# Performance work log

Hardware: AMD Instinct MI355X
Metric: run time of the kernel (lower is better)

Reference implementation:

```python
import jax, jax.numpy as jnp
import numpy as np

U, I, E, T = 60000, 30000, 64, 2000
N = U + I
ADJ_NNZ = 1_600_000
UI_NNZ = 800_000
TAGS_PER_ITEM = 4


def setup_inputs() -> dict:
    key = jax.random.key(0)
    ks = jax.random.split(key, 8)
    # LightGCN normalized adjacency in COO form (values already normalized offline)
    adj_rows = jax.random.randint(ks[0], (ADJ_NNZ,), 0, N, dtype=jnp.int32)
    adj_cols = jax.random.randint(ks[1], (ADJ_NNZ,), 0, N, dtype=jnp.int32)
    adj_vals = jax.random.uniform(ks[2], (ADJ_NNZ,), dtype=jnp.float32) * 0.01
    # Item-tag incidence H: 4 distinct tags per item (binary incidence, no duplicates)
    items_np = np.repeat(np.arange(I, dtype=np.int32), TAGS_PER_ITEM)
    tags_np = ((np.arange(I, dtype=np.int64)[:, None] * 7919 + np.arange(TAGS_PER_ITEM)[None, :] * 131) % T).astype(np.int32).reshape(-1)
    h_items = jnp.asarray(items_np)
    h_tags = jnp.asarray(tags_np)
    # Row-normalized user-item interaction matrix (D_u^-1 @ trn_mat) in COO form
    ui_rows = jax.random.randint(ks[3], (UI_NNZ,), 0, U, dtype=jnp.int32)
    ui_cols = jax.random.randint(ks[4], (UI_NNZ,), 0, I, dtype=jnp.int32)
    ui_vals = jax.random.uniform(ks[5], (UI_NNZ,), dtype=jnp.float32) * 0.01
    return {
        'user_embeds': jax.random.normal(ks[6], (U, E), dtype=jnp.float32) * 0.1,
        'item_embeds': jax.random.normal(jax.random.fold_in(ks[6], 1), (I, E), dtype=jnp.float32) * 0.1,
        'hypergraph_user_embeds': jax.random.normal(ks[7], (U, E), dtype=jnp.float32) * 0.1,
        'hypergraph_item_embeds': jax.random.normal(jax.random.fold_in(ks[7], 1), (I, E), dtype=jnp.float32) * 0.1,
        'adj_rows': adj_rows, 'adj_cols': adj_cols, 'adj_vals': adj_vals,
        'h_items': h_items, 'h_tags': h_tags,
        'ui_rows': ui_rows, 'ui_cols': ui_cols, 'ui_vals': ui_vals,
        'layer_num': 3,
    }


def _spmm(rows, cols, vals, x, n):
    # y[r] += vals[e] * x[cols[e]] for each edge e with rows[e]==r  (t.spmm)
    return jax.ops.segment_sum(vals[:, None] * x[cols], rows, num_segments=n)


def reference(user_embeds, item_embeds, hypergraph_user_embeds, hypergraph_item_embeds,
              adj_rows, adj_cols, adj_vals, h_items, h_tags, ui_rows, ui_cols, ui_vals,
              layer_num):
    ones = jnp.ones(h_items.shape[0], dtype=user_embeds.dtype)
    # B: hyperedge (tag) degree; D: item degree; zero degrees clamped to 1
    B = jax.ops.segment_sum(ones, h_tags, num_segments=T)
    D = jax.ops.segment_sum(ones, h_items, num_segments=I)
    B_inv = 1.0 / jnp.where(B == 0, 1.0, B)
    D_inv = 1.0 / jnp.where(D == 0, 1.0, D)

    def hconv(x):  # D^-1 H B^-1 H^T x, never materializing the item x item adjacency
        y = jax.ops.segment_sum(x[h_items], h_tags, num_segments=T) * B_inv[:, None]
        z = jax.ops.segment_sum(y[h_tags], h_items, num_segments=I)
        return z * D_inv[:, None]

    # LightGCN propagation: sum of all layer embeddings (layer 0 included)
    cur = jnp.concatenate([user_embeds, item_embeds], axis=0)  # [N, E]
    acc = cur
    for _ in range(layer_num):
        cur = _spmm(adj_rows, adj_cols, adj_vals, cur, N)
        acc = acc + cur

    # Hypergraph propagation on items
    hcur = hypergraph_item_embeds
    hacc = hcur
    for _ in range(layer_num):
        hcur = hconv(hcur)
        hacc = hacc + hcur

    # Hypergraph user embeds: own params + degree-normalized sum of interacted items
    hg_user = hypergraph_user_embeds + _spmm(ui_rows, ui_cols, ui_vals, hacc, U)

    return acc[:U], acc[U:], hg_user, hacc
```

## Files before the change

kernel.cpp:

```cpp
#include <hip/hip_runtime.h>

#define E 64
#define TQ 16
#define RPB 256
#define RPB_SHIFT 8
#define NBMAX 1024
#define CHUNK_C 4096
#define CHUNK_P 4096
#define FP8_SCALE 512.0f
#define FP8_INV   (1.0f / 512.0f)

static inline int nblk(long n, int bs) { return (int)((n + bs - 1) / bs); }


__device__ __forceinline__ unsigned short f2bf(float f) {
    unsigned u = __float_as_uint(f);
    u += 0x7FFF + ((u >> 16) & 1);
    return (unsigned short)(u >> 16);
}
__device__ __forceinline__ float bf2f(unsigned short h) {
    return __uint_as_float((unsigned)h << 16);
}
__device__ __forceinline__ int f2v15(float f) {
    unsigned u = __float_as_uint(f);
    u += 0x7FFF + ((u >> 16) & 1);
    return (int)((u >> 16) & 0x7FFF);
}
__device__ __forceinline__ float v15f(int p) {
    return __uint_as_float(((unsigned)p >> 17) << 16);
}
__device__ __forceinline__ int pack_fp8x4(float4 v) {
    int w = __builtin_amdgcn_cvt_pk_fp8_f32(v.x, v.y, 0, false);
    w = __builtin_amdgcn_cvt_pk_fp8_f32(v.z, v.w, w, true);
    return w;
}


__global__ void __launch_bounds__(512)
k_count_cvt(const int* __restrict__ adj_rows, int nadj,
            const int* __restrict__ ui_rows, int nui,
            const int* __restrict__ h_tags,
            int* __restrict__ bucket_cnt, int OFF_UI, int OFF_TAG, int NB, int ET,
            const float4* __restrict__ ua, const float4* __restrict__ ub,
            int splitv4, int* __restrict__ xf8, int ncvt, int CB) {
    __shared__ int h4[4][NBMAX];
    if ((int)blockIdx.x < CB) {
        for (int b = threadIdx.x; b < 4 * NBMAX; b += 512) ((int*)h4)[b] = 0;
        __syncthreads();
        int c = (threadIdx.x >> 4) & 3;
        int start = blockIdx.x * CHUNK_C;
        int end = start + CHUNK_C; if (end > ET) end = ET;
        for (int i = start + (int)threadIdx.x; i < end; i += 512) {
            int row;
            if (i < nadj) row = adj_rows[i];
            else if (i < nadj + nui) row = OFF_UI + ui_rows[i - nadj];
            else row = OFF_TAG + h_tags[i - nadj - nui];
            atomicAdd(&h4[c][row >> RPB_SHIFT], 1);
        }
        __syncthreads();
        for (int b = threadIdx.x; b < NB; b += 512) {
            int tot = h4[0][b] + h4[1][b] + h4[2][b] + h4[3][b];
            if (tot) atomicAdd(&bucket_cnt[b], tot);
        }
    } else {
        int i = ((int)blockIdx.x - CB) * 512 + threadIdx.x;
        if (i < ncvt) {
            float4 v = (i < splitv4) ? ua[i] : ub[i - splitv4];
            v.x *= FP8_SCALE; v.y *= FP8_SCALE; v.z *= FP8_SCALE; v.w *= FP8_SCALE;
            xf8[i] = pack_fp8x4(v);
        }
    }
}


__global__ void __launch_bounds__(1024)
k_scan_nb(const int* __restrict__ cnt, int* __restrict__ base, int* __restrict__ bcur,
          int* __restrict__ rp, int M, int NB, int ET) {
    __shared__ int sh[1024];
    int tid = threadIdx.x;
    int v = (tid < NB) ? cnt[tid] : 0;
    sh[tid] = v;
    __syncthreads();
    for (int off = 1; off < 1024; off <<= 1) {
        int t = (tid >= off) ? sh[tid - off] : 0;
        __syncthreads();
        sh[tid] += t;
        __syncthreads();
    }
    if (tid < NB) {
        int excl = sh[tid] - v;
        base[tid] = excl;
        bcur[tid] = excl;
        if (tid == NB - 1) base[NB] = sh[tid];
    }
    if (tid == 0) rp[M] = ET;
}


__global__ void __launch_bounds__(512)
k_partition(const int* __restrict__ adj_rows, const int* __restrict__ adj_cols,
            const float* __restrict__ adj_vals, int nadj,
            const int* __restrict__ ui_rows, const int* __restrict__ ui_cols,
            const float* __restrict__ ui_vals, int nui,
            const int* __restrict__ h_tags, const int* __restrict__ h_items,
            int* __restrict__ bcur, int2* __restrict__ staged,
            int OFF_UI, int OFF_TAG, int NB, int ET) {
    __shared__ int h4[4][NBMAX];
    for (int b = threadIdx.x; b < 4 * NBMAX; b += 512) ((int*)h4)[b] = 0;
    __syncthreads();

    int c = (threadIdx.x >> 4) & 3;
    int start = blockIdx.x * CHUNK_P;

    int rowA[8], colA[8], vbA[8];
    #pragma unroll
    for (int k = 0; k < 8; ++k) {
        int i = start + k * 512 + (int)threadIdx.x;
        int row = -1, col = 0, vb = 0;
        if (i < ET) {
            if (i < nadj) {
                row = adj_rows[i]; col = adj_cols[i]; vb = f2v15(adj_vals[i]);
            } else if (i < nadj + nui) {
                int j = i - nadj;
                row = OFF_UI + ui_rows[j]; col = ui_cols[j]; vb = f2v15(ui_vals[j]);
            } else {
                int j = i - nadj - nui;
                row = OFF_TAG + h_tags[j]; col = h_items[j]; vb = 0;
            }
            atomicAdd(&h4[c][row >> RPB_SHIFT], 1);
        }
        rowA[k] = row; colA[k] = col; vbA[k] = vb;
    }
    __syncthreads();

    for (int b = threadIdx.x; b < NB; b += 512) {
        int c0 = h4[0][b], c1 = h4[1][b], c2 = h4[2][b], c3 = h4[3][b];
        int tot = c0 + c1 + c2 + c3;
        if (tot) {
            int g = atomicAdd(&bcur[b], tot);
            h4[0][b] = g;
            h4[1][b] = g + c0;
            h4[2][b] = g + c0 + c1;
            h4[3][b] = g + c0 + c1 + c2;
        }
    }
    __syncthreads();

    #pragma unroll
    for (int k = 0; k < 8; ++k) {
        if (rowA[k] >= 0) {
            int b = rowA[k] >> RPB_SHIFT;
            int pos = atomicAdd(&h4[c][b], 1);
            staged[pos] = make_int2(((rowA[k] & (RPB - 1)) << 17) | colA[k], vbA[k]);
        }
    }
}


__global__ void __launch_bounds__(512)
k_bucket_csr(const int2* __restrict__ staged, const int* __restrict__ bbase,
             int* __restrict__ rp, int* __restrict__ pool, int M) {
    __shared__ int h4[4][RPB];
    __shared__ int scn[RPB];
    int b = blockIdx.x;
    int s0 = bbase[b], s1 = bbase[b + 1];
    for (int i = threadIdx.x; i < 4 * RPB; i += 512) ((int*)h4)[i] = 0;
    __syncthreads();
    int c = (threadIdx.x >> 4) & 3;
    for (int e = s0 + (int)threadIdx.x; e < s1; e += 512) {
        int lrow = ((unsigned)staged[e].x) >> 17;
        atomicAdd(&h4[c][lrow], 1);
    }
    __syncthreads();
    int tot = (threadIdx.x < RPB)
        ? h4[0][threadIdx.x] + h4[1][threadIdx.x] + h4[2][threadIdx.x] + h4[3][threadIdx.x] : 0;
    if (threadIdx.x < RPB) scn[threadIdx.x] = tot;
    __syncthreads();
    for (int off = 1; off < RPB; off <<= 1) {
        int t = 0;
        if (threadIdx.x < RPB && (int)threadIdx.x >= off) t = scn[threadIdx.x - off];
        __syncthreads();
        if (threadIdx.x < RPB) scn[threadIdx.x] += t;
        __syncthreads();
    }
    int row0 = b << RPB_SHIFT;
    if (threadIdx.x < RPB) {
        int excl = s0 + scn[threadIdx.x] - tot;
        if (row0 + (int)threadIdx.x < M) rp[row0 + threadIdx.x] = excl;
        int c0 = h4[0][threadIdx.x], c1 = h4[1][threadIdx.x], c2 = h4[2][threadIdx.x];
        h4[0][threadIdx.x] = excl;
        h4[1][threadIdx.x] = excl + c0;
        h4[2][threadIdx.x] = excl + c0 + c1;
        h4[3][threadIdx.x] = excl + c0 + c1 + c2;
    }
    __syncthreads();
    for (int e = s0 + (int)threadIdx.x; e < s1; e += 512) {
        int2 ed = staged[e];
        int lrow = ((unsigned)ed.x) >> 17;
        int pos = atomicAdd(&h4[c][lrow], 1);
        pool[pos] = (ed.y << 17) | (ed.x & 0x1FFFF);
    }
}


__device__ __forceinline__ void spmm_body(const int* __restrict__ rp,
                                          const int* __restrict__ pool,
                                          const int* __restrict__ xf8,
                                          int* __restrict__ yf8, int n, int bid) {
    int gid = bid * 256 + (int)threadIdx.x;
    int row = gid >> 4;
    if (row >= n) return;
    int q = gid & 15;
    int s0 = rp[row], s1 = rp[row + 1];
    float4 s = make_float4(0.f, 0.f, 0.f, 0.f);
    int e = s0;
    for (; e + 4 <= s1; e += 4) {
        int p0 = pool[e], p1 = pool[e + 1], p2 = pool[e + 2], p3 = pool[e + 3];
        int w0 = xf8[(long)(p0 & 0x1FFFF) * TQ + q];
        int w1 = xf8[(long)(p1 & 0x1FFFF) * TQ + q];
        int w2 = xf8[(long)(p2 & 0x1FFFF) * TQ + q];
        int w3 = xf8[(long)(p3 & 0x1FFFF) * TQ + q];
        float v0 = v15f(p0), v1 = v15f(p1), v2 = v15f(p2), v3 = v15f(p3);
        s.x += v0 * __builtin_amdgcn_cvt_f32_fp8(w0, 0);
        s.y += v0 * __builtin_amdgcn_cvt_f32_fp8(w0, 1);
        s.z += v0 * __builtin_amdgcn_cvt_f32_fp8(w0, 2);
        s.w += v0 * __builtin_amdgcn_cvt_f32_fp8(w0, 3);
        s.x += v1 * __builtin_amdgcn_cvt_f32_fp8(w1, 0);
        s.y += v1 * __builtin_amdgcn_cvt_f32_fp8(w1, 1);
        s.z += v1 * __builtin_amdgcn_cvt_f32_fp8(w1, 2);
        s.w += v1 * __builtin_amdgcn_cvt_f32_fp8(w1, 3);
        s.x += v2 * __builtin_amdgcn_cvt_f32_fp8(w2, 0);
        s.y += v2 * __builtin_amdgcn_cvt_f32_fp8(w2, 1);
        s.z += v2 * __builtin_amdgcn_cvt_f32_fp8(w2, 2);
        s.w += v2 * __builtin_amdgcn_cvt_f32_fp8(w2, 3);
        s.x += v3 * __builtin_amdgcn_cvt_f32_fp8(w3, 0);
        s.y += v3 * __builtin_amdgcn_cvt_f32_fp8(w3, 1);
        s.z += v3 * __builtin_amdgcn_cvt_f32_fp8(w3, 2);
        s.w += v3 * __builtin_amdgcn_cvt_f32_fp8(w3, 3);
    }
    for (; e < s1; ++e) {
        int p0 = pool[e];
        int w0 = xf8[(long)(p0 & 0x1FFFF) * TQ + q];
        float v0 = v15f(p0);
        s.x += v0 * __builtin_amdgcn_cvt_f32_fp8(w0, 0);
        s.y += v0 * __builtin_amdgcn_cvt_f32_fp8(w0, 1);
        s.z += v0 * __builtin_amdgcn_cvt_f32_fp8(w0, 2);
        s.w += v0 * __builtin_amdgcn_cvt_f32_fp8(w0, 3);
    }
    yf8[(long)row * TQ + q] = pack_fp8x4(s);
}

__device__ __forceinline__ void tag_hop_body(const int* __restrict__ rp, int rp_off,
                                             const int* __restrict__ pool,
                                             const float* __restrict__ x,
                                             float* __restrict__ y, int ntags, int bid) {
    int t = (bid * 256 + (int)threadIdx.x) >> 6;
    if (t >= ntags) return;
    int lane = threadIdx.x & 63;
    int q = lane & 15;
    int g = lane >> 4;
    int s0 = rp[rp_off + t], s1 = rp[rp_off + t + 1];
    float4 s = make_float4(0.f, 0.f, 0.f, 0.f);
    for (int e = s0 + g; e < s1; e += 4) {
        int it = pool[e] & 0x1FFFF;
        float4 xv = ((const float4*)x)[(long)it * TQ + q];
        s.x += xv.x; s.y += xv.y; s.z += xv.z; s.w += xv.w;
    }
    s.x += __shfl_xor(s.x, 16, 64); s.y += __shfl_xor(s.y, 16, 64);
    s.z += __shfl_xor(s.z, 16, 64); s.w += __shfl_xor(s.w, 16, 64);
    s.x += __shfl_xor(s.x, 32, 64); s.y += __shfl_xor(s.y, 32, 64);
    s.z += __shfl_xor(s.z, 32, 64); s.w += __shfl_xor(s.w, 32, 64);
    if (g == 0) {
        int b = s1 - s0;
        float binv = (b > 0) ? (1.f / (float)b) : 1.f;
        s.x *= binv; s.y *= binv; s.z *= binv; s.w *= binv;
        ((float4*)y)[(long)t * TQ + q] = s;
    }
}

__device__ __forceinline__ void tag_g_body(const int* __restrict__ rp, int rp_off,
                                           const int* __restrict__ pool,
                                           const int* __restrict__ tags, int K,
                                           const float* __restrict__ yin,
                                           const float* __restrict__ yprev,
                                           float* __restrict__ yout, int ntags, int bid) {
    int t = (bid * 256 + (int)threadIdx.x) >> 6;
    if (t >= ntags) return;
    int lane = threadIdx.x & 63;
    int q = lane & 15;
    int g = lane >> 4;
    int s0 = rp[rp_off + t], s1 = rp[rp_off + t + 1];
    float4 s = make_float4(0.f, 0.f, 0.f, 0.f);
    if (K == 4) {
        for (int e = s0 + g; e < s1; e += 4) {
            int it = pool[e] & 0x1FFFF;
            int4 t4 = ((const int4*)tags)[it];
            float4 a0 = ((const float4*)yin)[(long)t4.x * TQ + q];
            float4 a1 = ((const float4*)yin)[(long)t4.y * TQ + q];
            float4 a2 = ((const float4*)yin)[(long)t4.z * TQ + q];
            float4 a3 = ((const float4*)yin)[(long)t4.w * TQ + q];
            s.x += (a0.x + a1.x) + (a2.x + a3.x);
            s.y += (a0.y + a1.y) + (a2.y + a3.y);
            s.z += (a0.z + a1.z) + (a2.z + a3.z);
            s.w += (a0.w + a1.w) + (a2.w + a3.w);
        }
    } else {
        for (int e = s0 + g; e < s1; e += 4) {
            int it = pool[e] & 0x1FFFF;
            for (int k = 0; k < K; ++k) {
                int tt = tags[(long)it * K + k];
                float4 a = ((const float4*)yin)[(long)tt * TQ + q];
                s.x += a.x; s.y += a.y; s.z += a.z; s.w += a.w;
            }
        }
    }
    s.x += __shfl_xor(s.x, 16, 64); s.y += __shfl_xor(s.y, 16, 64);
    s.z += __shfl_xor(s.z, 16, 64); s.w += __shfl_xor(s.w, 16, 64);
    s.x += __shfl_xor(s.x, 32, 64); s.y += __shfl_xor(s.y, 32, 64);
    s.z += __shfl_xor(s.z, 32, 64); s.w += __shfl_xor(s.w, 32, 64);
    if (g == 0) {
        int b = s1 - s0;
        float dinv = 1.f / (float)K;
        float f = (b > 0) ? (dinv / (float)b) : 0.f;
        s.x *= f; s.y *= f; s.z *= f; s.w *= f;
        long o = (long)t * TQ + q;
        if (yprev) {
            float4 p1 = ((const float4*)yprev)[o];
            float4 p2 = ((const float4*)yin)[o];
            s.x += p1.x + p2.x; s.y += p1.y + p2.y;
            s.z += p1.z + p2.z; s.w += p1.w + p2.w;
        }
        ((float4*)yout)[o] = s;
    }
}

__device__ __forceinline__ void items_body(const int* __restrict__ tags, int K,
                                           const float* __restrict__ ysum,
                                           const float* __restrict__ init,
                                           float* __restrict__ hacc,
                                           ushort4* __restrict__ hacc_bf,
                                           int nitems, int bid) {
    int gid = bid * 256 + (int)threadIdx.x;
    int i = gid >> 4;
    if (i >= nitems) return;
    int q = gid & 15;
    float4 s = make_float4(0.f, 0.f, 0.f, 0.f);
    if (K == 4) {
        int4 t4 = ((const int4*)tags)[i];
        float4 y0 = ((const float4*)ysum)[(long)t4.x * TQ + q];
        float4 y1 = ((const float4*)ysum)[(long)t4.y * TQ + q];
        float4 y2 = ((const float4*)ysum)[(long)t4.z * TQ + q];
        float4 y3 = ((const float4*)ysum)[(long)t4.w * TQ + q];
        s.x = (y0.x + y1.x) + (y2.x + y3.x);
        s.y = (y0.y + y1.y) + (y2.y + y3.y);
        s.z = (y0.z + y1.z) + (y2.z + y3.z);
        s.w = (y0.w + y1.w) + (y2.w + y3.w);
    } else {
        for (int k = 0; k < K; ++k) {
            int tt = tags[(long)i * K + k];
            float4 yv = ((const float4*)ysum)[(long)tt * TQ + q];
            s.x += yv.x; s.y += yv.y; s.z += yv.z; s.w += yv.w;
        }
    }
    float dinv = 1.f / (float)K;
    s.x *= dinv; s.y *= dinv; s.z *= dinv; s.w *= dinv;
    long o = (long)i * TQ + q;
    float4 a = ((const float4*)init)[o];
    a.x += s.x; a.y += s.y; a.z += s.z; a.w += s.w;
    ((float4*)hacc)[o] = a;
    ushort4 hb;
    hb.x = f2bf(a.x); hb.y = f2bf(a.y); hb.z = f2bf(a.z); hb.w = f2bf(a.w);
    hacc_bf[o] = hb;
}


__global__ void __launch_bounds__(256)
k_spmm_tag(const int* __restrict__ rp, const int* __restrict__ pool,
           const int* __restrict__ xf8, int* __restrict__ yf8, int n, int SB,
           int rp_off, const float* __restrict__ xtag, float* __restrict__ y1,
           int ntags) {
    if ((int)blockIdx.x < SB)
        spmm_body(rp, pool, xf8, yf8, n, blockIdx.x);
    else
        tag_hop_body(rp, rp_off, pool, xtag, y1, ntags, (int)blockIdx.x - SB);
}

__global__ void __launch_bounds__(256)
k_spmm_g(const int* __restrict__ rp, const int* __restrict__ pool,
         const int* __restrict__ xf8, int* __restrict__ yf8, int n, int SB,
         int rp_off, const int* __restrict__ tags, int K,
         const float* __restrict__ yin, const float* __restrict__ yprev,
         float* __restrict__ yout, int ntags) {
    if ((int)blockIdx.x < SB)
        spmm_body(rp, pool, xf8, yf8, n, blockIdx.x);
    else
        tag_g_body(rp, rp_off, pool, tags, K, yin, yprev, yout, ntags,
                   (int)blockIdx.x - SB);
}

__global__ void __launch_bounds__(256)
k_final_items(const float4* __restrict__ ua, const float4* __restrict__ ub,
              int splitv4, const int* __restrict__ l1, const int* __restrict__ l2,
              const int* __restrict__ l3, float4* __restrict__ acc, int n4, int FSB,
              const int* __restrict__ tags, int K, const float* __restrict__ ysum,
              const float* __restrict__ hyper_item, float* __restrict__ hacc,
              ushort4* __restrict__ hacc_bf, int nitems) {
    if ((int)blockIdx.x < FSB) {
        int i = (int)blockIdx.x * 256 + threadIdx.x;
        if (i >= n4) return;
        float4 a = (i < splitv4) ? ua[i] : ub[i - splitv4];
        int w1 = l1[i], w2 = l2[i], w3 = l3[i];
        a.x += (__builtin_amdgcn_cvt_f32_fp8(w1, 0) + __builtin_amdgcn_cvt_f32_fp8(w2, 0)
                + __builtin_amdgcn_cvt_f32_fp8(w3, 0)) * FP8_INV;
        a.y += (__builtin_amdgcn_cvt_f32_fp8(w1, 1) + __builtin_amdgcn_cvt_f32_fp8(w2, 1)
                + __builtin_amdgcn_cvt_f32_fp8(w3, 1)) * FP8_INV;
        a.z += (__builtin_amdgcn_cvt_f32_fp8(w1, 2) + __builtin_amdgcn_cvt_f32_fp8(w2, 2)
                + __builtin_amdgcn_cvt_f32_fp8(w3, 2)) * FP8_INV;
        a.w += (__builtin_amdgcn_cvt_f32_fp8(w1, 3) + __builtin_amdgcn_cvt_f32_fp8(w2, 3)
                + __builtin_amdgcn_cvt_f32_fp8(w3, 3)) * FP8_INV;
        acc[i] = a;
    } else {
        items_body(tags, K, ysum, hyper_item, hacc, hacc_bf, nitems,
                   (int)blockIdx.x - FSB);
    }
}


__global__ void k_csr_spmm_base_bf(const int* __restrict__ rp, int rp_off,
                                   const int* __restrict__ pool,
                                   const ushort4* __restrict__ xbf,
                                   const float* __restrict__ base,
                                   float* __restrict__ out, int n) {
    int gid = blockIdx.x * blockDim.x + threadIdx.x;
    int row = gid >> 4;
    if (row >= n) return;
    int q = gid & 15;
    int s0 = rp[rp_off + row], s1 = rp[rp_off + row + 1];
    float4 s = make_float4(0.f, 0.f, 0.f, 0.f);
    int e = s0;
    for (; e + 4 <= s1; e += 4) {
        int p0 = pool[e], p1 = pool[e + 1], p2 = pool[e + 2], p3 = pool[e + 3];
        ushort4 h0 = xbf[(long)(p0 & 0x1FFFF) * TQ + q];
        ushort4 h1 = xbf[(long)(p1 & 0x1FFFF) * TQ + q];
        ushort4 h2 = xbf[(long)(p2 & 0x1FFFF) * TQ + q];
        ushort4 h3 = xbf[(long)(p3 & 0x1FFFF) * TQ + q];
        float v0 = v15f(p0), v1 = v15f(p1), v2 = v15f(p2), v3 = v15f(p3);
        s.x += v0 * bf2f(h0.x); s.y += v0 * bf2f(h0.y);
        s.z += v0 * bf2f(h0.z); s.w += v0 * bf2f(h0.w);
        s.x += v1 * bf2f(h1.x); s.y += v1 * bf2f(h1.y);
        s.z += v1 * bf2f(h1.z); s.w += v1 * bf2f(h1.w);
        s.x += v2 * bf2f(h2.x); s.y += v2 * bf2f(h2.y);
        s.z += v2 * bf2f(h2.z); s.w += v2 * bf2f(h2.w);
        s.x += v3 * bf2f(h3.x); s.y += v3 * bf2f(h3.y);
        s.z += v3 * bf2f(h3.z); s.w += v3 * bf2f(h3.w);
    }
    for (; e < s1; ++e) {
        int p0 = pool[e];
        ushort4 h0 = xbf[(long)(p0 & 0x1FFFF) * TQ + q];
        float v0 = v15f(p0);
        s.x += v0 * bf2f(h0.x); s.y += v0 * bf2f(h0.y);
        s.z += v0 * bf2f(h0.z); s.w += v0 * bf2f(h0.w);
    }
    long o = (long)row * TQ + q;
    float4 bv = ((const float4*)base)[o];
    bv.x += s.x; bv.y += s.y; bv.z += s.z; bv.w += s.w;
    ((float4*)out)[o] = bv;
}


extern "C" void kernel_launch(void* const* d_in, const int* in_sizes, int n_in,
                              void* d_out, int out_size, void* d_ws, size_t ws_size,
                              hipStream_t stream) {
    const float* user_embeds = (const float*)d_in[0];
    const float* item_embeds = (const float*)d_in[1];
    const float* hyper_user  = (const float*)d_in[2];
    const float* hyper_item  = (const float*)d_in[3];
    const int*   adj_rows    = (const int*)d_in[4];
    const int*   adj_cols    = (const int*)d_in[5];
    const float* adj_vals    = (const float*)d_in[6];
    const int*   h_items     = (const int*)d_in[7];
    const int*   h_tags      = (const int*)d_in[8];
    const int*   ui_rows     = (const int*)d_in[9];
    const int*   ui_cols     = (const int*)d_in[10];
    const float* ui_vals     = (const float*)d_in[11];

    const int U = in_sizes[0] / E;
    const int I = in_sizes[1] / E;
    const int N = U + I;
    const int ADJ = in_sizes[4];
    const int NH  = in_sizes[7];
    const int UI  = in_sizes[9];
    const int K   = NH / I;
    const int T   = 2000;
    const int ET  = ADJ + UI + NH;

    const int OFF_UI  = (N + RPB - 1) & ~(RPB - 1);
    const int OFF_TAG = (OFF_UI + U + RPB - 1) & ~(RPB - 1);
    const int M   = OFF_TAG + T;
    const int NB  = (M + RPB - 1) >> RPB_SHIFT;

    float* out     = (float*)d_out;
    float* acc     = out;
    float* hg_user = out + (size_t)N * E;
    float* hacc    = hg_user + (size_t)U * E;

    char* ws = (char*)d_ws;
    auto alloc = [&](size_t bytes) { char* p = ws; ws += (bytes + 255) & ~(size_t)255; return p; };

    int*  xf0 = (int*)alloc((size_t)N * TQ * sizeof(int));
    int*  xf1 = (int*)alloc((size_t)N * TQ * sizeof(int));
    int*  xf2 = (int*)alloc((size_t)N * TQ * sizeof(int));
    int*  xf3 = (int*)alloc((size_t)N * TQ * sizeof(int));
    int2* staged = (int2*)alloc((size_t)ET * sizeof(int2));
    float* y1      = (float*)alloc((size_t)T * E * sizeof(float));
    float* y2      = (float*)alloc((size_t)T * E * sizeof(float));
    float* ys      = (float*)alloc((size_t)T * E * sizeof(float));
    unsigned short* hacc_bf = (unsigned short*)alloc((size_t)I * E * sizeof(unsigned short));
    int*   pool    = (int*)alloc((size_t)ET * sizeof(int));
    int*   rp      = (int*)alloc((size_t)(M + 1) * sizeof(int));
    int*   bcnt    = (int*)alloc((size_t)NBMAX * sizeof(int));
    int*   bbase   = (int*)alloc((size_t)(NBMAX + 1) * sizeof(int));
    int*   bcur    = (int*)alloc((size_t)NBMAX * sizeof(int));

    const int BS = 256;
    const int TAG_BLOCKS = nblk((long)T * 64, 256);
    const int CB  = nblk(ET, CHUNK_C);
    const int CVB = nblk((long)N * TQ, 512);
    const int SB  = nblk((long)N * TQ, BS);
    const int FSB = nblk((long)N * TQ, BS);
    const int IB  = nblk((long)I * TQ, BS);

    hipMemsetAsync(bcnt, 0, (size_t)NB * sizeof(int), stream);
    k_count_cvt<<<CB + CVB, 512, 0, stream>>>(
        adj_rows, ADJ, ui_rows, UI, h_tags, bcnt, OFF_UI, OFF_TAG, NB, ET,
        (const float4*)user_embeds, (const float4*)item_embeds, U * TQ,
        xf0, N * TQ, CB);
    k_scan_nb<<<1, 1024, 0, stream>>>(bcnt, bbase, bcur, rp, M, NB, ET);
    k_partition<<<nblk(ET, CHUNK_P), 512, 0, stream>>>(
        adj_rows, adj_cols, adj_vals, ADJ, ui_rows, ui_cols, ui_vals, UI,
        h_tags, h_items, bcur, staged, OFF_UI, OFF_TAG, NB, ET);
    k_bucket_csr<<<NB, 512, 0, stream>>>(staged, bbase, rp, pool, M);

    k_spmm_tag<<<SB + TAG_BLOCKS, BS, 0, stream>>>(
        rp, pool, xf0, xf1, N, SB, OFF_TAG, hyper_item, y1, T);
    k_spmm_g<<<SB + TAG_BLOCKS, BS, 0, stream>>>(
        rp, pool, xf1, xf2, N, SB, OFF_TAG, h_tags, K, y1, nullptr, y2, T);
    k_spmm_g<<<SB + TAG_BLOCKS, BS, 0, stream>>>(
        rp, pool, xf2, xf3, N, SB, OFF_TAG, h_tags, K, y2, y1, ys, T);

    k_final_items<<<FSB + IB, BS, 0, stream>>>(
        (const float4*)user_embeds, (const float4*)item_embeds, U * TQ,
        xf1, xf2, xf3, (float4*)acc, N * TQ, FSB,
        h_tags, K, ys, hyper_item, hacc, (ushort4*)hacc_bf, I);

    k_csr_spmm_base_bf<<<nblk((long)U * TQ, BS), BS, 0, stream>>>(
        rp, OFF_UI, pool, (const ushort4*)hacc_bf, hyper_user, hg_user, U);
}
```

Measured before the change: 333.8 us.

## Fuse final LightGCN layer with accumulation and unroll gather loops by eight

The third adjacency SpMM layer now accumulates the input embeddings plus the two earlier FP8 layers and its own fp32 result straight into the output. This removes the xf3 intermediate and its write and re-read in a separate final kernel. The item hypergraph step becomes its own kernel. The FP8 and BF16 gather loops are also unrolled to eight edges to keep more loads in flight, at the cost of higher register pressure. The last layer now stays in fp32 instead of being rounded through FP8, which slightly changes the numerics.

Result: no change. 331.8 us (-0.6%).

```diff
diff --git a/kernel.cpp b/kernel.cpp
--- a/kernel.cpp
+++ b/kernel.cpp
@@ -203,6 +203,50 @@
 }
 
 
+#define FP8_ACC(ss, ww, vv)                                               \
+    ss.x += vv * __builtin_amdgcn_cvt_f32_fp8(ww, 0);                     \
+    ss.y += vv * __builtin_amdgcn_cvt_f32_fp8(ww, 1);                     \
+    ss.z += vv * __builtin_amdgcn_cvt_f32_fp8(ww, 2);                     \
+    ss.w += vv * __builtin_amdgcn_cvt_f32_fp8(ww, 3);
+
+__device__ __forceinline__ float4 spmm_sum(const int* __restrict__ pool,
+                                           const int* __restrict__ xf8,
+                                           int s0, int s1, int q) {
+    float4 s = make_float4(0.f, 0.f, 0.f, 0.f);
+    int e = s0;
+    for (; e + 8 <= s1; e += 8) {
+        int p0 = pool[e],     p1 = pool[e + 1], p2 = pool[e + 2], p3 = pool[e + 3];
+        int p4 = pool[e + 4], p5 = pool[e + 5], p6 = pool[e + 6], p7 = pool[e + 7];
+        int w0 = xf8[(long)(p0 & 0x1FFFF) * TQ + q];
+        int w1 = xf8[(long)(p1 & 0x1FFFF) * TQ + q];
+        int w2 = xf8[(long)(p2 & 0x1FFFF) * TQ + q];
+        int w3 = xf8[(long)(p3 & 0x1FFFF) * TQ + q];
+        int w4 = xf8[(long)(p4 & 0x1FFFF) * TQ + q];
+        int w5 = xf8[(long)(p5 & 0x1FFFF) * TQ + q];
+        int w6 = xf8[(long)(p6 & 0x1FFFF) * TQ + q];
+        int w7 = xf8[(long)(p7 & 0x1FFFF) * TQ + q];
+        FP8_ACC(s, w0, v15f(p0)); FP8_ACC(s, w1, v15f(p1));
+        FP8_ACC(s, w2, v15f(p2)); FP8_ACC(s, w3, v15f(p3));
+        FP8_ACC(s, w4, v15f(p4)); FP8_ACC(s, w5, v15f(p5));
+        FP8_ACC(s, w6, v15f(p6)); FP8_ACC(s, w7, v15f(p7));
+    }
+    for (; e + 4 <= s1; e += 4) {
+        int p0 = pool[e], p1 = pool[e + 1], p2 = pool[e + 2], p3 = pool[e + 3];
+        int w0 = xf8[(long)(p0 & 0x1FFFF) * TQ + q];
+        int w1 = xf8[(long)(p1 & 0x1FFFF) * TQ + q];
+        int w2 = xf8[(long)(p2 & 0x1FFFF) * TQ + q];
+        int w3 = xf8[(long)(p3 & 0x1FFFF) * TQ + q];
+        FP8_ACC(s, w0, v15f(p0)); FP8_ACC(s, w1, v15f(p1));
+        FP8_ACC(s, w2, v15f(p2)); FP8_ACC(s, w3, v15f(p3));
+    }
+    for (; e < s1; ++e) {
+        int p0 = pool[e];
+        int w0 = xf8[(long)(p0 & 0x1FFFF) * TQ + q];
+        FP8_ACC(s, w0, v15f(p0));
+    }
+    return s;
+}
+
 __device__ __forceinline__ void spmm_body(const int* __restrict__ rp,
                                           const int* __restrict__ pool,
                                           const int* __restrict__ xf8,
@@ -211,43 +255,35 @@
     int row = gid >> 4;
     if (row >= n) return;
     int q = gid & 15;
-    int s0 = rp[row], s1 = rp[row + 1];
-    float4 s = make_float4(0.f, 0.f, 0.f, 0.f);
-    int e = s0;
-    for (; e + 4 <= s1; e += 4) {
-        int p0 = pool[e], p1 = pool[e + 1], p2 = pool[e + 2], p3 = pool[e + 3];
-        int w0 = xf8[(long)(p0 & 0x1FFFF) * TQ + q];
-        int w1 = xf8[(long)(p1 & 0x1FFFF) * TQ + q];
-        int w2 = xf8[(long)(p2 & 0x1FFFF) * TQ + q];
-        int w3 = xf8[(long)(p3 & 0x1FFFF) * TQ + q];
-        float v0 = v15f(p0), v1 = v15f(p1), v2 = v15f(p2), v3 = v15f(p3);
-        s.x += v0 * __builtin_amdgcn_cvt_f32_fp8(w0, 0);
-        s.y += v0 * __builtin_amdgcn_cvt_f32_fp8(w0, 1);
-        s.z += v0 * __builtin_amdgcn_cvt_f32_fp8(w0, 2);
-        s.w += v0 * __builtin_amdgcn_cvt_f32_fp8(w0, 3);
-        s.x += v1 * __builtin_amdgcn_cvt_f32_fp8(w1, 0);
-        s.y += v1 * __builtin_amdgcn_cvt_f32_fp8(w1, 1);
-        s.z += v1 * __builtin_amdgcn_cvt_f32_fp8(w1, 2);
-        s.w += v1 * __builtin_amdgcn_cvt_f32_fp8(w1, 3);
-        s.x += v2 * __builtin_amdgcn_cvt_f32_fp8(w2, 0);
-        s.y += v2 * __builtin_amdgcn_cvt_f32_fp8(w2, 1);
-        s.z += v2 * __builtin_amdgcn_cvt_f32_fp8(w2, 2);
-        s.w += v2 * __builtin_amdgcn_cvt_f32_fp8(w2, 3);
-        s.x += v3 * __builtin_amdgcn_cvt_f32_fp8(w3, 0);
-        s.y += v3 * __builtin_amdgcn_cvt_f32_fp8(w3, 1);
-        s.z += v3 * __builtin_amdgcn_cvt_f32_fp8(w3, 2);
-        s.w += v3 * __builtin_amdgcn_cvt_f32_fp8(w3, 3);
-    }
-    for (; e < s1; ++e) {
-        int p0 = pool[e];
-        int w0 = xf8[(long)(p0 & 0x1FFFF) * TQ + q];
-        float v0 = v15f(p0);
-        s.x += v0 * __builtin_amdgcn_cvt_f32_fp8(w0, 0);
-        s.y += v0 * __builtin_amdgcn_cvt_f32_fp8(w0, 1);
-        s.z += v0 * __builtin_amdgcn_cvt_f32_fp8(w0, 2);
-        s.w += v0 * __builtin_amdgcn_cvt_f32_fp8(w0, 3);
-    }
+    float4 s = spmm_sum(pool, xf8, rp[row], rp[row + 1], q);
     yf8[(long)row * TQ + q] = pack_fp8x4(s);
+}
+
+__device__ __forceinline__ void spmm_acc_body(const int* __restrict__ rp,
+                                              const int* __restrict__ pool,
+                                              const int* __restrict__ xf8,
+                                              const int* __restrict__ l1,
+                                              const int* __restrict__ l2,
+                                              const float4* __restrict__ ua,
+                                              const float4* __restrict__ ub,
+                                              int splitv4, float4* __restrict__ acc,
+                                              int n, int bid) {
+    int gid = bid * 256 + (int)threadIdx.x;
+    int row = gid >> 4;
+    if (row >= n) return;
+    int q = gid & 15;
+    float4 s = spmm_sum(pool, xf8, rp[row], rp[row + 1], q);
+    float4 a = (gid < splitv4) ? ua[gid] : ub[gid - splitv4];
+    int w1 = l1[gid], w2 = l2[gid];
+    a.x += (__builtin_amdgcn_cvt_f32_fp8(w1, 0) + __builtin_amdgcn_cvt_f32_fp8(w2, 0)
+            + s.x) * FP8_INV;
+    a.y += (__builtin_amdgcn_cvt_f32_fp8(w1, 1) + __builtin_amdgcn_cvt_f32_fp8(w2, 1)
+            + s.y) * FP8_INV;
+    a.z += (__builtin_amdgcn_cvt_f32_fp8(w1, 2) + __builtin_amdgcn_cvt_f32_fp8(w2, 2)
+            + s.z) * FP8_INV;
+    a.w += (__builtin_amdgcn_cvt_f32_fp8(w1, 3) + __builtin_amdgcn_cvt_f32_fp8(w2, 3)
+            + s.w) * FP8_INV;
+    acc[gid] = a;
 }
 
 __device__ __forceinline__ void tag_hop_body(const int* __restrict__ rp, int rp_off,
@@ -334,13 +370,52 @@
     }
 }
 
-__device__ __forceinline__ void items_body(const int* __restrict__ tags, int K,
-                                           const float* __restrict__ ysum,
-                                           const float* __restrict__ init,
-                                           float* __restrict__ hacc,
-                                           ushort4* __restrict__ hacc_bf,
-                                           int nitems, int bid) {
-    int gid = bid * 256 + (int)threadIdx.x;
+
+__global__ void __launch_bounds__(256)
+k_spmm_tag(const int* __restrict__ rp, const int* __restrict__ pool,
+           const int* __restrict__ xf8, int* __restrict__ yf8, int n, int SB,
+           int rp_off, const float* __restrict__ xtag, float* __restrict__ y1,
+           int ntags) {
+    if ((int)blockIdx.x < SB)
+        spmm_body(rp, pool, xf8, yf8, n, blockIdx.x);
+    else
+        tag_hop_body(rp, rp_off, pool, xtag, y1, ntags, (int)blockIdx.x - SB);
+}
+
+__global__ void __launch_bounds__(256)
+k_spmm_g(const int* __restrict__ rp, const int* __restrict__ pool,
+         const int* __restrict__ xf8, int* __restrict__ yf8, int n, int SB,
+         int rp_off, const int* __restrict__ tags, int K,
+         const float* __restrict__ yin, const float* __restrict__ yprev,
+         float* __restrict__ yout, int ntags) {
+    if ((int)blockIdx.x < SB)
+        spmm_body(rp, pool, xf8, yf8, n, blockIdx.x);
+    else
+        tag_g_body(rp, rp_off, pool, tags, K, yin, yprev, yout, ntags,
+                   (int)blockIdx.x - SB);
+}
+
+__global__ void __launch_bounds__(256)
+k_spmm_final(const int* __restrict__ rp, const int* __restrict__ pool,
+             const int* __restrict__ xf8, const int* __restrict__ l1,
+             const int* __restrict__ l2,
+             const float4* __restrict__ ua, const float4* __restrict__ ub,
+             int splitv4, float4* __restrict__ acc, int n, int SB,
+             int rp_off, const int* __restrict__ tags, int K,
+             const float* __restrict__ yin, const float* __restrict__ yprev,
+             float* __restrict__ yout, int ntags) {
+    if ((int)blockIdx.x < SB)
+        spmm_acc_body(rp, pool, xf8, l1, l2, ua, ub, splitv4, acc, n, blockIdx.x);
+    else
+        tag_g_body(rp, rp_off, pool, tags, K, yin, yprev, yout, ntags,
+                   (int)blockIdx.x - SB);
+}
+
+__global__ void __launch_bounds__(256)
+k_items(const int* __restrict__ tags, int K, const float* __restrict__ ysum,
+        const float* __restrict__ init, float* __restrict__ hacc,
+        ushort4* __restrict__ hacc_bf, int nitems) {
+    int gid = blockIdx.x * 256 + (int)threadIdx.x;
     int i = gid >> 4;
     if (i >= nitems) return;
     int q = gid & 15;
@@ -374,57 +449,9 @@
 }
 
 
-__global__ void __launch_bounds__(256)
-k_spmm_tag(const int* __restrict__ rp, const int* __restrict__ pool,
-           const int* __restrict__ xf8, int* __restrict__ yf8, int n, int SB,
-           int rp_off, const float* __restrict__ xtag, float* __restrict__ y1,
-           int ntags) {
-    if ((int)blockIdx.x < SB)
-        spmm_body(rp, pool, xf8, yf8, n, blockIdx.x);
-    else
-        tag_hop_body(rp, rp_off, pool, xtag, y1, ntags, (int)blockIdx.x - SB);
-}
-
-__global__ void __launch_bounds__(256)
-k_spmm_g(const int* __restrict__ rp, const int* __restrict__ pool,
-         const int* __restrict__ xf8, int* __restrict__ yf8, int n, int SB,
-         int rp_off, const int* __restrict__ tags, int K,
-         const float* __restrict__ yin, const float* __restrict__ yprev,
-         float* __restrict__ yout, int ntags) {
-    if ((int)blockIdx.x < SB)
-        spmm_body(rp, pool, xf8, yf8, n, blockIdx.x);
-    else
-        tag_g_body(rp, rp_off, pool, tags, K, yin, yprev, yout, ntags,
-                   (int)blockIdx.x - SB);
-}
-
-__global__ void __launch_bounds__(256)
-k_final_items(const float4* __restrict__ ua, const float4* __restrict__ ub,
-              int splitv4, const int* __restrict__ l1, const int* __restrict__ l2,
-              const int* __restrict__ l3, float4* __restrict__ acc, int n4, int FSB,
-              const int* __restrict__ tags, int K, const float* __restrict__ ysum,
-              const float* __restrict__ hyper_item, float* __restrict__ hacc,
-              ushort4* __restrict__ hacc_bf, int nitems) {
-    if ((int)blockIdx.x < FSB) {
-        int i = (int)blockIdx.x * 256 + threadIdx.x;
-        if (i >= n4) return;
-        float4 a = (i < splitv4) ? ua[i] : ub[i - splitv4];
-        int w1 = l1[i], w2 = l2[i], w3 = l3[i];
-        a.x += (__builtin_amdgcn_cvt_f32_fp8(w1, 0) + __builtin_amdgcn_cvt_f32_fp8(w2, 0)
-                + __builtin_amdgcn_cvt_f32_fp8(w3, 0)) * FP8_INV;
-        a.y += (__builtin_amdgcn_cvt_f32_fp8(w1, 1) + __builtin_amdgcn_cvt_f32_fp8(w2, 1)
-                + __builtin_amdgcn_cvt_f32_fp8(w3, 1)) * FP8_INV;
-        a.z += (__builtin_amdgcn_cvt_f32_fp8(w1, 2) + __builtin_amdgcn_cvt_f32_fp8(w2, 2)
-                + __builtin_amdgcn_cvt_f32_fp8(w3, 2)) * FP8_INV;
-        a.w += (__builtin_amdgcn_cvt_f32_fp8(w1, 3) + __builtin_amdgcn_cvt_f32_fp8(w2, 3)
-                + __builtin_amdgcn_cvt_f32_fp8(w3, 3)) * FP8_INV;
-        acc[i] = a;
-    } else {
-        items_body(tags, K, ysum, hyper_item, hacc, hacc_bf, nitems,
-                   (int)blockIdx.x - FSB);
-    }
-}
-
+#define BF_ACC(ss, hh, vv)                                                \
+    ss.x += vv * bf2f(hh.x); ss.y += vv * bf2f(hh.y);                     \
+    ss.z += vv * bf2f(hh.z); ss.w += vv * bf2f(hh.w);
 
 __global__ void k_csr_spmm_base_bf(const int* __restrict__ rp, int rp_off,
                                    const int* __restrict__ pool,
@@ -438,28 +465,35 @@
     int s0 = rp[rp_off + row], s1 = rp[rp_off + row + 1];
     float4 s = make_float4(0.f, 0.f, 0.f, 0.f);
     int e = s0;
+    for (; e + 8 <= s1; e += 8) {
+        int p0 = pool[e],     p1 = pool[e + 1], p2 = pool[e + 2], p3 = pool[e + 3];
+        int p4 = pool[e + 4], p5 = pool[e + 5], p6 = pool[e + 6], p7 = pool[e + 7];
+        ushort4 h0 = xbf[(long)(p0 & 0x1FFFF) * TQ + q];
+        ushort4 h1 = xbf[(long)(p1 & 0x1FFFF) * TQ + q];
+        ushort4 h2 = xbf[(long)(p2 & 0x1FFFF) * TQ + q];
+        ushort4 h3 = xbf[(long)(p3 & 0x1FFFF) * TQ + q];
+        ushort4 h4 = xbf[(long)(p4 & 0x1FFFF) * TQ + q];
+        ushort4 h5 = xbf[(long)(p5 & 0x1FFFF) * TQ + q];
+        ushort4 h6 = xbf[(long)(p6 & 0x1FFFF) * TQ + q];
+        ushort4 h7 = xbf[(long)(p7 & 0x1FFFF) * TQ + q];
+        BF_ACC(s, h0, v15f(p0)); BF_ACC(s, h1, v15f(p1));
+        BF_ACC(s, h2, v15f(p2)); BF_ACC(s, h3, v15f(p3));
+        BF_ACC(s, h4, v15f(p4)); BF_ACC(s, h5, v15f(p5));
+        BF_ACC(s, h6, v15f(p6)); BF_ACC(s, h7, v15f(p7));
+    }
     for (; e + 4 <= s1; e += 4) {
         int p0 = pool[e], p1 = pool[e + 1], p2 = pool[e + 2], p3 = pool[e + 3];
         ushort4 h0 = xbf[(long)(p0 & 0x1FFFF) * TQ + q];
         ushort4 h1 = xbf[(long)(p1 & 0x1FFFF) * TQ + q];
         ushort4 h2 = xbf[(long)(p2 & 0x1FFFF) * TQ + q];
         ushort4 h3 = xbf[(long)(p3 & 0x1FFFF) * TQ + q];
-        float v0 = v15f(p0), v1 = v15f(p1), v2 = v15f(p2), v3 = v15f(p3);
-        s.x += v0 * bf2f(h0.x); s.y += v0 * bf2f(h0.y);
-        s.z += v0 * bf2f(h0.z); s.w += v0 * bf2f(h0.w);
-        s.x += v1 * bf2f(h1.x); s.y += v1 * bf2f(h1.y);
-        s.z += v1 * bf2f(h1.z); s.w += v1 * bf2f(h1.w);
-        s.x += v2 * bf2f(h2.x); s.y += v2 * bf2f(h2.y);
-        s.z += v2 * bf2f(h2.z); s.w += v2 * bf2f(h2.w);
-        s.x += v3 * bf2f(h3.x); s.y += v3 * bf2f(h3.y);
-        s.z += v3 * bf2f(h3.z); s.w += v3 * bf2f(h3.w);
+        BF_ACC(s, h0, v15f(p0)); BF_ACC(s, h1, v15f(p1));
+        BF_ACC(s, h2, v15f(p2)); BF_ACC(s, h3, v15f(p3));
     }
     for (; e < s1; ++e) {
         int p0 = pool[e];
         ushort4 h0 = xbf[(long)(p0 & 0x1FFFF) * TQ + q];
-        float v0 = v15f(p0);
-        s.x += v0 * bf2f(h0.x); s.y += v0 * bf2f(h0.y);
-        s.z += v0 * bf2f(h0.z); s.w += v0 * bf2f(h0.w);
+        BF_ACC(s, h0, v15f(p0));
     }
     long o = (long)row * TQ + q;
     float4 bv = ((const float4*)base)[o];
@@ -510,7 +544,6 @@
     int*  xf0 = (int*)alloc((size_t)N * TQ * sizeof(int));
     int*  xf1 = (int*)alloc((size_t)N * TQ * sizeof(int));
     int*  xf2 = (int*)alloc((size_t)N * TQ * sizeof(int));
-    int*  xf3 = (int*)alloc((size_t)N * TQ * sizeof(int));
     int2* staged = (int2*)alloc((size_t)ET * sizeof(int2));
     float* y1      = (float*)alloc((size_t)T * E * sizeof(float));
     float* y2      = (float*)alloc((size_t)T * E * sizeof(float));
@@ -527,7 +560,6 @@
     const int CB  = nblk(ET, CHUNK_C);
     const int CVB = nblk((long)N * TQ, 512);
     const int SB  = nblk((long)N * TQ, BS);
-    const int FSB = nblk((long)N * TQ, BS);
     const int IB  = nblk((long)I * TQ, BS);
 
     hipMemsetAsync(bcnt, 0, (size_t)NB * sizeof(int), stream);
@@ -545,12 +577,12 @@
         rp, pool, xf0, xf1, N, SB, OFF_TAG, hyper_item, y1, T);
     k_spmm_g<<<SB + TAG_BLOCKS, BS, 0, stream>>>(
         rp, pool, xf1, xf2, N, SB, OFF_TAG, h_tags, K, y1, nullptr, y2, T);
-    k_spmm_g<<<SB + TAG_BLOCKS, BS, 0, stream>>>(
-        rp, pool, xf2, xf3, N, SB, OFF_TAG, h_tags, K, y2, y1, ys, T);
-
-    k_final_items<<<FSB + IB, BS, 0, stream>>>(
+    k_spmm_final<<<SB + TAG_BLOCKS, BS, 0, stream>>>(
+        rp, pool, xf2, xf1, xf2,
         (const float4*)user_embeds, (const float4*)item_embeds, U * TQ,
-        xf1, xf2, xf3, (float4*)acc, N * TQ, FSB,
+        (float4*)acc, N, SB, OFF_TAG, h_tags, K, y2, y1, ys, T);
+
+    k_items<<<IB, BS, 0, stream>>>(
         h_tags, K, ys, hyper_item, hacc, (ushort4*)hacc_bf, I);
 
     k_csr_spmm_base_bf<<<nblk((long)U * TQ, BS), BS, 0, stream>>>(
```
